# Performance work log

Measured on AMD Instinct MI355X. Metric: run time of the kernel, lower is better.

The kernel has to match this reference:

```python
import jax, jax.numpy as jnp
import numpy as np

N = 100000
E = 1600000


def _gcn_conv(x, src, dst, norm, W, b, n_nodes):
    # PyG GCNConv: h = x @ W; aggregate normalized messages; add bias.
    h = x @ W                                   # [N, C_out]
    msg = h[src] * norm[:, None]                # [E', C_out] gathered messages
    out = jax.ops.segment_sum(msg, dst, num_segments=n_nodes)
    return out + b


def _norm_coeffs(src, dst, n_nodes):
    # symmetric normalization with self-loops: D^{-1/2} (A+I) D^{-1/2}
    ones = jnp.ones(src.shape[0], dtype=jnp.float32)
    deg = jax.ops.segment_sum(ones, dst, num_segments=n_nodes)
    dis = jnp.where(deg > 0, jax.lax.rsqrt(jnp.maximum(deg, 1.0)), 0.0)
    return dis[src] * dis[dst]


def setup_inputs() -> dict:
    key = jax.random.key(0)
    k1, k2, k3, k4 = jax.random.split(key, 4)
    x = jax.random.normal(k1, (N, 128), dtype=jnp.float32)
    edge_index = jax.random.randint(k2, (2, E), 0, N, dtype=jnp.int64)
    W1 = jax.random.normal(k3, (128, 128), dtype=jnp.float32) * (1.0 / np.sqrt(128))
    b1 = jnp.zeros((128,), dtype=jnp.float32)
    W2 = jax.random.normal(k4, (128, 64), dtype=jnp.float32) * (1.0 / np.sqrt(128))
    b2 = jnp.zeros((64,), dtype=jnp.float32)
    return {"x": x, "edge_index": edge_index, "W1": W1, "b1": b1, "W2": W2, "b2": b2}


def reference(x, edge_index, W1, b1, W2, b2):
    n_nodes = x.shape[0]
    loop = jnp.arange(n_nodes, dtype=edge_index.dtype)
    src = jnp.concatenate([edge_index[0], loop])   # add self-loops
    dst = jnp.concatenate([edge_index[1], loop])
    norm = _norm_coeffs(src, dst, n_nodes)
    h = _gcn_conv(x, src, dst, norm, W1, b1, n_nodes)
    h = jax.nn.relu(h)
    # dropout(p=0.2) is identity in eval mode
    out = _gcn_conv(h, src, dst, norm, W2, b2, n_nodes)
    return out
```

## Files before the change

kernel.cpp:

```cpp
#include <hip/hip_runtime.h>
#include <hip/hip_bf16.h>


typedef short short8v __attribute__((ext_vector_type(8)));
typedef float f32x4   __attribute__((ext_vector_type(4)));

#define BSHIFT 9
#define BSIZE  512
#define CAPSH  14
#define CAP    (1 << CAPSH)

__device__ __forceinline__ short f2bf(float f) {
    unsigned u = __float_as_uint(f);
    return (short)((u + 0x7fffu + ((u >> 16) & 1u)) >> 16);
}
__device__ __forceinline__ float bfbits(unsigned short s) {
    return __uint_as_float((unsigned)s << 16);
}
__device__ __forceinline__ unsigned pack2bf(float a, float b) {
    return (unsigned)(unsigned short)f2bf(a) | ((unsigned)(unsigned short)f2bf(b) << 16);
}

__global__ void k_init(int* __restrict__ bcur, int nbuck) {
    int i = threadIdx.x;
    if (i < nbuck) bcur[i] = i << CAPSH;
}

__global__ __launch_bounds__(256) void k_bucket(const int* __restrict__ src,
                                                const int* __restrict__ dst,
                                                int* __restrict__ bcur,
                                                int2* __restrict__ ebuf,
                                                int E, int nbuck) {
    __shared__ int sdst[4096];
    __shared__ int ssrc[4096];
    __shared__ int hist[256];
    __shared__ int base[256];
    int t = threadIdx.x;
    int e0 = blockIdx.x * 4096;
    for (int i = t; i < nbuck; i += 256) hist[i] = 0;
    for (int i = 0; i < 16; ++i) {
        int k = i * 256 + t;
        int e = e0 + k;
        sdst[k] = (e < E) ? dst[e] : -1;
        ssrc[k] = (e < E) ? src[e] : 0;
    }
    __syncthreads();
    for (int i = 0; i < 16; ++i) {
        int d = sdst[i * 256 + t];
        if (d >= 0) atomicAdd(&hist[d >> BSHIFT], 1);
    }
    __syncthreads();
    for (int b = t; b < nbuck; b += 256) {
        int c = hist[b];
        base[b] = c ? atomicAdd(&bcur[b], c) : 0;
        hist[b] = 0;
    }
    __syncthreads();
    for (int i = 0; i < 16; ++i) {
        int k = i * 256 + t;
        int d = sdst[k];
        if (d >= 0) {
            int bk = d >> BSHIFT;
            int off = atomicAdd(&hist[bk], 1);
            ebuf[base[bk] + off] = make_int2(ssrc[k], d);
        }
    }
}

__global__ __launch_bounds__(BSIZE) void k_bdeg(const int2* __restrict__ ebuf,
                                                const int* __restrict__ bcur,
                                                int* __restrict__ deg,
                                                int* __restrict__ row_ptr,
                                                float* __restrict__ dinv, int n) {
    __shared__ int hist[BSIZE];
    __shared__ int s[BSIZE];
    int b = blockIdx.x;
    int t = threadIdx.x;
    hist[t] = 0;
    __syncthreads();
    int base = b << CAPSH;
    int cnt  = bcur[b] - base;
    int lo = b << BSHIFT;
    for (int k = t; k < cnt; k += BSIZE)
        atomicAdd(&hist[ebuf[base + k].y - lo], 1);
    __syncthreads();
    int v = hist[t];
    s[t] = v;
    __syncthreads();
    for (int off = 1; off < BSIZE; off <<= 1) {
        int add = (t >= off) ? s[t - off] : 0;
        __syncthreads();
        s[t] += add;
        __syncthreads();
    }
    int node = lo + t;
    if (node < n) {
        deg[node]     = v;
        row_ptr[node] = base + s[t] - v;
        dinv[node]    = rsqrtf((float)(v + 1));
    }
}

__global__ __launch_bounds__(BSIZE) void k_bscatter(const int2* __restrict__ ebuf,
                                                    const int* __restrict__ bcur,
                                                    const int* __restrict__ row_ptr,
                                                    const float* __restrict__ dinv,
                                                    int2* __restrict__ csr8, int n) {
    __shared__ int cur[BSIZE];
    int b = blockIdx.x;
    int t = threadIdx.x;
    int lo = b << BSHIFT;
    int node = lo + t;
    cur[t] = (node < n) ? row_ptr[node] : 0;
    __syncthreads();
    int base = b << CAPSH;
    int cnt  = bcur[b] - base;
    for (int k = t; k < cnt; k += BSIZE) {
        int2 ed = ebuf[base + k];
        int pos = atomicAdd(&cur[ed.y - lo], 1);
        csr8[pos] = make_int2(ed.x, __float_as_int(dinv[ed.x]));
    }
}

__global__ void k_prepW(const float* __restrict__ W1, const float* __restrict__ W2,
                        short* __restrict__ w1t, short* __restrict__ w2t) {
    int i = blockIdx.x * blockDim.x + threadIdx.x;
    if (i < 128 * 128) {
        int n = i >> 7, k = i & 127;
        w1t[i] = f2bf(W1[k * 128 + n]);
    } else if (i < 128 * 128 + 64 * 128) {
        int j = i - 128 * 128;
        int n = j >> 7, k = j & 127;
        w2t[j] = f2bf(W2[k * 64 + n]);
    }
}

#define LDP 136
__global__ __launch_bounds__(256) void k_gemm1(const float* __restrict__ x,
                                               const short* __restrict__ w1t,
                                               short* __restrict__ h, int nrows) {
    __shared__ short xs[64 * LDP];
    __shared__ short wt[128 * LDP];
    int t = threadIdx.x;
    int row0 = blockIdx.x * 64;
    for (int i = 0; i < 16; ++i) {
        int idx = t + i * 256;
        int r = idx >> 5, c4 = idx & 31;
        float4 v = make_float4(0.f, 0.f, 0.f, 0.f);
        if (row0 + r < nrows) v = ((const float4*)x)[(size_t)(row0 + r) * 32 + c4];
        short4 o = make_short4(f2bf(v.x), f2bf(v.y), f2bf(v.z), f2bf(v.w));
        *(short4*)&xs[r * LDP + c4 * 4] = o;
    }
    for (int i = 0; i < 16; ++i) {
        int idx = t + i * 256;
        int n = idx >> 5, c4 = idx & 31;
        *(short4*)&wt[n * LDP + c4 * 4] = ((const short4*)w1t)[idx];
    }
    __syncthreads();
    int wave = t >> 6, lane = t & 63;
    int quad = lane >> 4, c = lane & 15;
    int m0 = wave * 16;
    f32x4 acc[8] = {};
    #pragma unroll
    for (int kc = 0; kc < 4; ++kc) {
        short8v a = *(const short8v*)&xs[(m0 + c) * LDP + kc * 32 + quad * 8];
        #pragma unroll
        for (int nt = 0; nt < 8; ++nt) {
            short8v b = *(const short8v*)&wt[(nt * 16 + c) * LDP + kc * 32 + quad * 8];
            acc[nt] = __builtin_amdgcn_mfma_f32_16x16x32_bf16(a, b, acc[nt], 0, 0, 0);
        }
    }
    #pragma unroll
    for (int nt = 0; nt < 8; ++nt)
        #pragma unroll
        for (int r = 0; r < 4; ++r) {
            int row = row0 + m0 + quad * 4 + r;
            if (row < nrows) h[(size_t)row * 128 + nt * 16 + c] = f2bf(acc[nt][r]);
        }
}

__global__ __launch_bounds__(256) void k_gemm2(const unsigned* __restrict__ aggb,
                                               const float* __restrict__ b1,
                                               const short* __restrict__ w2t,
                                               short* __restrict__ h2, int nrows) {
    __shared__ short xs[64 * LDP];
    __shared__ short wt[64 * LDP];
    int t = threadIdx.x;
    int row0 = blockIdx.x * 64;
    for (int i = 0; i < 16; ++i) {
        int idx = t + i * 256;
        int r = idx >> 6, cp = idx & 63;
        unsigned o = 0;
        if (row0 + r < nrows) {
            unsigned u = aggb[(size_t)(row0 + r) * 64 + cp];
            float2 bb = ((const float2*)b1)[cp];
            float vx = fmaxf(__uint_as_float(u << 16) + bb.x, 0.f);
            float vy = fmaxf(__uint_as_float(u & 0xffff0000u) + bb.y, 0.f);
            o = pack2bf(vx, vy);
        }
        *(unsigned*)&xs[r * LDP + cp * 2] = o;
    }
    for (int i = 0; i < 8; ++i) {
        int idx = t + i * 256;
        int n = idx >> 5, c4 = idx & 31;
        *(short4*)&wt[n * LDP + c4 * 4] = ((const short4*)w2t)[idx];
    }
    __syncthreads();
    int wave = t >> 6, lane = t & 63;
    int quad = lane >> 4, c = lane & 15;
    int m0 = wave * 16;
    f32x4 acc[4] = {};
    #pragma unroll
    for (int kc = 0; kc < 4; ++kc) {
        short8v av = *(const short8v*)&xs[(m0 + c) * LDP + kc * 32 + quad * 8];
        #pragma unroll
        for (int nt = 0; nt < 4; ++nt) {
            short8v b = *(const short8v*)&wt[(nt * 16 + c) * LDP + kc * 32 + quad * 8];
            acc[nt] = __builtin_amdgcn_mfma_f32_16x16x32_bf16(av, b, acc[nt], 0, 0, 0);
        }
    }
    #pragma unroll
    for (int nt = 0; nt < 4; ++nt)
        #pragma unroll
        for (int r = 0; r < 4; ++r) {
            int row = row0 + m0 + quad * 4 + r;
            if (row < nrows) h2[(size_t)row * 64 + nt * 16 + c] = f2bf(acc[nt][r]);
        }
}

__global__ __launch_bounds__(256) void k_pull128(const unsigned short* __restrict__ h,
                                                 const int* __restrict__ row_ptr,
                                                 const int* __restrict__ deg,
                                                 const int2* __restrict__ csr8,
                                                 const float* __restrict__ dinv,
                                                 unsigned* __restrict__ aggb, int n) {
    int wave = (blockIdx.x * 256 + threadIdx.x) >> 6;
    int lane = threadIdx.x & 63;
    if (wave >= n) return;
    int i = __builtin_amdgcn_readfirstlane(wave);
    float di = dinv[i];
    float2 acc;
    {
        unsigned u = ((const unsigned*)(h + (size_t)i * 128))[lane];
        float w = di * di;
        acc.x = __uint_as_float(u << 16) * w;
        acc.y = __uint_as_float(u & 0xffff0000u) * w;
    }
    int beg = row_ptr[i];
    int cnt = deg[i];
    int k = 0;
    for (; k + 8 <= cnt; k += 8) {
        int2 e[8];
        unsigned u[8];
        #pragma unroll
        for (int j = 0; j < 8; ++j) e[j] = csr8[beg + k + j];
        #pragma unroll
        for (int j = 0; j < 8; ++j)
            u[j] = ((const unsigned*)(h + (size_t)e[j].x * 128))[lane];
        #pragma unroll
        for (int j = 0; j < 8; ++j) {
            float nr = di * __int_as_float(e[j].y);
            acc.x += __uint_as_float(u[j] << 16) * nr;
            acc.y += __uint_as_float(u[j] & 0xffff0000u) * nr;
        }
    }
    for (; k < cnt; ++k) {
        int2 e = csr8[beg + k];
        float nr = di * __int_as_float(e.y);
        unsigned u = ((const unsigned*)(h + (size_t)e.x * 128))[lane];
        acc.x += __uint_as_float(u << 16) * nr;
        acc.y += __uint_as_float(u & 0xffff0000u) * nr;
    }
    aggb[(size_t)i * 64 + lane] = pack2bf(acc.x, acc.y);
}

__global__ __launch_bounds__(256) void k_pull64(const unsigned short* __restrict__ h,
                                                const int* __restrict__ row_ptr,
                                                const int* __restrict__ deg,
                                                const int2* __restrict__ csr8,
                                                const float* __restrict__ dinv,
                                                const float* __restrict__ b2,
                                                float* __restrict__ out, int n) {
    int wave = (blockIdx.x * 256 + threadIdx.x) >> 6;
    int lane = threadIdx.x & 63;
    if (wave >= n) return;
    int i = __builtin_amdgcn_readfirstlane(wave);
    float di = dinv[i];
    float acc = bfbits(h[(size_t)i * 64 + lane]) * di * di;
    int beg = row_ptr[i];
    int cnt = deg[i];
    int k = 0;
    for (; k + 8 <= cnt; k += 8) {
        int2 e[8];
        unsigned short u[8];
        #pragma unroll
        for (int j = 0; j < 8; ++j) e[j] = csr8[beg + k + j];
        #pragma unroll
        for (int j = 0; j < 8; ++j) u[j] = h[(size_t)e[j].x * 64 + lane];
        #pragma unroll
        for (int j = 0; j < 8; ++j)
            acc += bfbits(u[j]) * (di * __int_as_float(e[j].y));
    }
    for (; k < cnt; ++k) {
        int2 e = csr8[beg + k];
        acc += bfbits(h[(size_t)e.x * 64 + lane]) * (di * __int_as_float(e.y));
    }
    out[(size_t)i * 64 + lane] = acc + b2[lane];
}

extern "C" void kernel_launch(void* const* d_in, const int* in_sizes, int n_in,
                              void* d_out, int out_size, void* d_ws, size_t ws_size,
                              hipStream_t stream) {
    const float* x  = (const float*)d_in[0];
    const int*   ei = (const int*)d_in[1];
    const float* W1 = (const float*)d_in[2];
    const float* b1 = (const float*)d_in[3];
    const float* W2 = (const float*)d_in[4];
    const float* b2 = (const float*)d_in[5];
    float* out = (float*)d_out;

    const int N = in_sizes[0] / 128;
    const int E = in_sizes[1] / 2;
    const int* src = ei;
    const int* dst = ei + E;
    const int nbuck = (N + BSIZE - 1) >> BSHIFT;
    const size_t capE = (size_t)nbuck << CAPSH;

    float* dinv    = (float*)d_ws;
    int*   deg     = (int*)(dinv + N);
    int*   row_ptr = deg + N;
    int*   bcur    = row_ptr + N;
    short* w1t     = (short*)(bcur + 256);
    short* w2t     = w1t + 128 * 128;
    int2*  csr8    = (int2*)(w2t + 64 * 128);
    short* bufH    = (short*)(csr8 + capE);
    short* bufH2   = bufH + (size_t)N * 128;
    unsigned* aggb = (unsigned*)(bufH2 + (size_t)N * 64);
    int2*  ebuf    = (int2*)bufH2;

    const int ntile = (E + 4095) / 4096;

    k_init<<<1, 256, 0, stream>>>(bcur, nbuck);
    k_bucket<<<ntile, 256, 0, stream>>>(src, dst, bcur, ebuf, E, nbuck);
    k_bdeg<<<nbuck, BSIZE, 0, stream>>>(ebuf, bcur, deg, row_ptr, dinv, N);
    k_bscatter<<<nbuck, BSIZE, 0, stream>>>(ebuf, bcur, row_ptr, dinv, csr8, N);

    k_prepW<<<96, 256, 0, stream>>>(W1, W2, w1t, w2t);

    k_gemm1<<<(N + 63) / 64, 256, 0, stream>>>(x, w1t, bufH, N);
    k_pull128<<<(N + 3) / 4, 256, 0, stream>>>((const unsigned short*)bufH, row_ptr, deg, csr8, dinv, aggb, N);

    k_gemm2<<<(N + 63) / 64, 256, 0, stream>>>(aggb, b1, w2t, bufH2, N);
    k_pull64<<<(N + 3) / 4, 256, 0, stream>>>((const unsigned short*)bufH2, row_ptr, deg, csr8, dinv, b2, out, N);
}
```

Baseline: 304.5 us.

## Pack edges to 32-bit, fuse CSR build in LDS, look up dinv at pull time

Bucketed edges are now packed into one 32-bit word (source shifted left, plus the local destination), which halves bucket-buffer traffic. The degree and scatter kernels are merged into one kernel that caches each bucket's edges in 64KB of shared memory, so the second global read of the bucket disappears. CSR entries shrink from int2 to a plain source index, and the pull kernels gather dinv[src] with an extra dependent load. Weight prep and bucket-cursor init are merged into a single launch. The costs are higher shared-memory use, which lowers occupancy in the CSR kernel, and an extra random gather per edge in both aggregations.

Measured after the change: 306.9 us. About the same (+0.8%).

```diff
diff --git a/kernel.cpp b/kernel.cpp
--- a/kernel.cpp
+++ b/kernel.cpp
@@ -14,22 +14,36 @@
     unsigned u = __float_as_uint(f);
     return (short)((u + 0x7fffu + ((u >> 16) & 1u)) >> 16);
 }
-__device__ __forceinline__ float bfbits(unsigned short s) {
-    return __uint_as_float((unsigned)s << 16);
-}
 __device__ __forceinline__ unsigned pack2bf(float a, float b) {
     return (unsigned)(unsigned short)f2bf(a) | ((unsigned)(unsigned short)f2bf(b) << 16);
 }
-
-__global__ void k_init(int* __restrict__ bcur, int nbuck) {
-    int i = threadIdx.x;
-    if (i < nbuck) bcur[i] = i << CAPSH;
+__device__ __forceinline__ float bflo(unsigned u) { return __uint_as_float(u << 16); }
+__device__ __forceinline__ float bfhi(unsigned u) { return __uint_as_float(u & 0xffff0000u); }
+
+__global__ void k_prep(const float* __restrict__ W1, const float* __restrict__ W2,
+                       short* __restrict__ w1t, short* __restrict__ w2t,
+                       int* __restrict__ bcur, int nbuck) {
+    int b = blockIdx.x;
+    int t = threadIdx.x;
+    if (b == gridDim.x - 1) {
+        if (t < nbuck) bcur[t] = t << CAPSH;
+        return;
+    }
+    int i = b * 256 + t;
+    if (i < 128 * 128) {
+        int n = i >> 7, k = i & 127;
+        w1t[i] = f2bf(W1[k * 128 + n]);
+    } else {
+        int j = i - 128 * 128;
+        int n = j >> 7, k = j & 127;
+        w2t[j] = f2bf(W2[k * 64 + n]);
+    }
 }
 
 __global__ __launch_bounds__(256) void k_bucket(const int* __restrict__ src,
                                                 const int* __restrict__ dst,
                                                 int* __restrict__ bcur,
-                                                int2* __restrict__ ebuf,
+                                                unsigned* __restrict__ ebuf,
                                                 int E, int nbuck) {
     __shared__ int sdst[4096];
     __shared__ int ssrc[4096];
@@ -62,18 +76,21 @@
         if (d >= 0) {
             int bk = d >> BSHIFT;
             int off = atomicAdd(&hist[bk], 1);
-            ebuf[base[bk] + off] = make_int2(ssrc[k], d);
-        }
-    }
-}
-
-__global__ __launch_bounds__(BSIZE) void k_bdeg(const int2* __restrict__ ebuf,
+            ebuf[base[bk] + off] = ((unsigned)ssrc[k] << BSHIFT) | (unsigned)(d & (BSIZE - 1));
+        }
+    }
+}
+
+__global__ __launch_bounds__(BSIZE) void k_bcsr(const unsigned* __restrict__ ebuf,
                                                 const int* __restrict__ bcur,
                                                 int* __restrict__ deg,
                                                 int* __restrict__ row_ptr,
-                                                float* __restrict__ dinv, int n) {
+                                                float* __restrict__ dinv,
+                                                unsigned* __restrict__ csr4, int n) {
+    __shared__ unsigned edges[CAP];
     __shared__ int hist[BSIZE];
     __shared__ int s[BSIZE];
+    __shared__ int cur[BSIZE];
     int b = blockIdx.x;
     int t = threadIdx.x;
     hist[t] = 0;
@@ -81,8 +98,11 @@
     int base = b << CAPSH;
     int cnt  = bcur[b] - base;
     int lo = b << BSHIFT;
-    for (int k = t; k < cnt; k += BSIZE)
-        atomicAdd(&hist[ebuf[base + k].y - lo], 1);
+    for (int k = t; k < cnt; k += BSIZE) {
+        unsigned e = ebuf[base + k];
+        edges[k] = e;
+        atomicAdd(&hist[e & (BSIZE - 1)], 1);
+    }
     __syncthreads();
     int v = hist[t];
     s[t] = v;
@@ -93,45 +113,19 @@
         s[t] += add;
         __syncthreads();
     }
+    int rp = base + s[t] - v;
+    cur[t] = rp;
     int node = lo + t;
     if (node < n) {
         deg[node]     = v;
-        row_ptr[node] = base + s[t] - v;
+        row_ptr[node] = rp;
         dinv[node]    = rsqrtf((float)(v + 1));
     }
-}
-
-__global__ __launch_bounds__(BSIZE) void k_bscatter(const int2* __restrict__ ebuf,
-                                                    const int* __restrict__ bcur,
-                                                    const int* __restrict__ row_ptr,
-                                                    const float* __restrict__ dinv,
-                                                    int2* __restrict__ csr8, int n) {
-    __shared__ int cur[BSIZE];
-    int b = blockIdx.x;
-    int t = threadIdx.x;
-    int lo = b << BSHIFT;
-    int node = lo + t;
-    cur[t] = (node < n) ? row_ptr[node] : 0;
-    __syncthreads();
-    int base = b << CAPSH;
-    int cnt  = bcur[b] - base;
+    __syncthreads();
     for (int k = t; k < cnt; k += BSIZE) {
-        int2 ed = ebuf[base + k];
-        int pos = atomicAdd(&cur[ed.y - lo], 1);
-        csr8[pos] = make_int2(ed.x, __float_as_int(dinv[ed.x]));
-    }
-}
-
-__global__ void k_prepW(const float* __restrict__ W1, const float* __restrict__ W2,
-                        short* __restrict__ w1t, short* __restrict__ w2t) {
-    int i = blockIdx.x * blockDim.x + threadIdx.x;
-    if (i < 128 * 128) {
-        int n = i >> 7, k = i & 127;
-        w1t[i] = f2bf(W1[k * 128 + n]);
-    } else if (i < 128 * 128 + 64 * 128) {
-        int j = i - 128 * 128;
-        int n = j >> 7, k = j & 127;
-        w2t[j] = f2bf(W2[k * 64 + n]);
+        unsigned e = edges[k];
+        int pos = atomicAdd(&cur[e & (BSIZE - 1)], 1);
+        csr4[pos] = e >> BSHIFT;
     }
 }
 
@@ -194,8 +188,8 @@
         if (row0 + r < nrows) {
             unsigned u = aggb[(size_t)(row0 + r) * 64 + cp];
             float2 bb = ((const float2*)b1)[cp];
-            float vx = fmaxf(__uint_as_float(u << 16) + bb.x, 0.f);
-            float vy = fmaxf(__uint_as_float(u & 0xffff0000u) + bb.y, 0.f);
+            float vx = fmaxf(bflo(u) + bb.x, 0.f);
+            float vy = fmaxf(bfhi(u) + bb.y, 0.f);
             o = pack2bf(vx, vy);
         }
         *(unsigned*)&xs[r * LDP + cp * 2] = o;
@@ -231,7 +225,7 @@
 __global__ __launch_bounds__(256) void k_pull128(const unsigned short* __restrict__ h,
                                                  const int* __restrict__ row_ptr,
                                                  const int* __restrict__ deg,
-                                                 const int2* __restrict__ csr8,
+                                                 const unsigned* __restrict__ csr4,
                                                  const float* __restrict__ dinv,
                                                  unsigned* __restrict__ aggb, int n) {
     int wave = (blockIdx.x * 256 + threadIdx.x) >> 6;
@@ -243,33 +237,36 @@
     {
         unsigned u = ((const unsigned*)(h + (size_t)i * 128))[lane];
         float w = di * di;
-        acc.x = __uint_as_float(u << 16) * w;
-        acc.y = __uint_as_float(u & 0xffff0000u) * w;
+        acc.x = bflo(u) * w;
+        acc.y = bfhi(u) * w;
     }
     int beg = row_ptr[i];
     int cnt = deg[i];
     int k = 0;
     for (; k + 8 <= cnt; k += 8) {
-        int2 e[8];
-        unsigned u[8];
-        #pragma unroll
-        for (int j = 0; j < 8; ++j) e[j] = csr8[beg + k + j];
+        unsigned sid[8];
+        float ds[8];
+        unsigned g[8];
+        #pragma unroll
+        for (int j = 0; j < 8; ++j) sid[j] = csr4[beg + k + j];
+        #pragma unroll
+        for (int j = 0; j < 8; ++j) ds[j] = dinv[sid[j]];
         #pragma unroll
         for (int j = 0; j < 8; ++j)
-            u[j] = ((const unsigned*)(h + (size_t)e[j].x * 128))[lane];
+            g[j] = ((const unsigned*)(h + (size_t)sid[j] * 128))[lane];
         #pragma unroll
         for (int j = 0; j < 8; ++j) {
-            float nr = di * __int_as_float(e[j].y);
-            acc.x += __uint_as_float(u[j] << 16) * nr;
-            acc.y += __uint_as_float(u[j] & 0xffff0000u) * nr;
+            float nr = di * ds[j];
+            acc.x += bflo(g[j]) * nr;
+            acc.y += bfhi(g[j]) * nr;
         }
     }
     for (; k < cnt; ++k) {
-        int2 e = csr8[beg + k];
-        float nr = di * __int_as_float(e.y);
-        unsigned u = ((const unsigned*)(h + (size_t)e.x * 128))[lane];
-        acc.x += __uint_as_float(u << 16) * nr;
-        acc.y += __uint_as_float(u & 0xffff0000u) * nr;
+        unsigned sid = csr4[beg + k];
+        float nr = di * dinv[sid];
+        unsigned g = ((const unsigned*)(h + (size_t)sid * 128))[lane];
+        acc.x += bflo(g) * nr;
+        acc.y += bfhi(g) * nr;
     }
     aggb[(size_t)i * 64 + lane] = pack2bf(acc.x, acc.y);
 }
@@ -277,7 +274,7 @@
 __global__ __launch_bounds__(256) void k_pull64(const unsigned short* __restrict__ h,
                                                 const int* __restrict__ row_ptr,
                                                 const int* __restrict__ deg,
-                                                const int2* __restrict__ csr8,
+                                                const unsigned* __restrict__ csr4,
                                                 const float* __restrict__ dinv,
                                                 const float* __restrict__ b2,
                                                 float* __restrict__ out, int n) {
@@ -286,24 +283,31 @@
     if (wave >= n) return;
     int i = __builtin_amdgcn_readfirstlane(wave);
     float di = dinv[i];
-    float acc = bfbits(h[(size_t)i * 64 + lane]) * di * di;
+    float acc = bflo((unsigned)h[(size_t)i * 64 + lane] << 16 >> 16 << 16) * 0.0f;
+    {
+        unsigned u = h[(size_t)i * 64 + lane];
+        acc = __uint_as_float(u << 16) * di * di;
+    }
     int beg = row_ptr[i];
     int cnt = deg[i];
     int k = 0;
     for (; k + 8 <= cnt; k += 8) {
-        int2 e[8];
+        unsigned sid[8];
+        float ds[8];
         unsigned short u[8];
         #pragma unroll
-        for (int j = 0; j < 8; ++j) e[j] = csr8[beg + k + j];
-        #pragma unroll
-        for (int j = 0; j < 8; ++j) u[j] = h[(size_t)e[j].x * 64 + lane];
+        for (int j = 0; j < 8; ++j) sid[j] = csr4[beg + k + j];
+        #pragma unroll
+        for (int j = 0; j < 8; ++j) ds[j] = dinv[sid[j]];
+        #pragma unroll
+        for (int j = 0; j < 8; ++j) u[j] = h[(size_t)sid[j] * 64 + lane];
         #pragma unroll
         for (int j = 0; j < 8; ++j)
-            acc += bfbits(u[j]) * (di * __int_as_float(e[j].y));
+            acc += __uint_as_float((unsigned)u[j] << 16) * (di * ds[j]);
     }
     for (; k < cnt; ++k) {
-        int2 e = csr8[beg + k];
-        acc += bfbits(h[(size_t)e.x * 64 + lane]) * (di * __int_as_float(e.y));
+        unsigned sid = csr4[beg + k];
+        acc += __uint_as_float((unsigned)h[(size_t)sid * 64 + lane] << 16) * (di * dinv[sid]);
     }
     out[(size_t)i * 64 + lane] = acc + b2[lane];
 }
@@ -326,30 +330,28 @@
     const int nbuck = (N + BSIZE - 1) >> BSHIFT;
     const size_t capE = (size_t)nbuck << CAPSH;
 
-    float* dinv    = (float*)d_ws;
-    int*   deg     = (int*)(dinv + N);
-    int*   row_ptr = deg + N;
-    int*   bcur    = row_ptr + N;
-    short* w1t     = (short*)(bcur + 256);
-    short* w2t     = w1t + 128 * 128;
-    int2*  csr8    = (int2*)(w2t + 64 * 128);
-    short* bufH    = (short*)(csr8 + capE);
-    short* bufH2   = bufH + (size_t)N * 128;
-    unsigned* aggb = (unsigned*)(bufH2 + (size_t)N * 64);
-    int2*  ebuf    = (int2*)bufH2;
+    float* dinv     = (float*)d_ws;
+    int*   deg      = (int*)(dinv + N);
+    int*   row_ptr  = deg + N;
+    int*   bcur     = row_ptr + N;
+    short* w1t      = (short*)(bcur + 256);
+    short* w2t      = w1t + 128 * 128;
+    unsigned* csr4  = (unsigned*)(w2t + 64 * 128);
+    short* bufH     = (short*)(csr4 + capE);
+    short* bufH2    = bufH + (size_t)N * 128;
+    unsigned* aggb  = (unsigned*)(bufH2 + (size_t)N * 64);
+    unsigned* ebuf  = (unsigned*)bufH2;
 
     const int ntile = (E + 4095) / 4096;
 
-    k_init<<<1, 256, 0, stream>>>(bcur, nbuck);
+    k_prep<<<97, 256, 0, stream>>>(W1, W2, w1t, w2t, bcur, nbuck);
+
     k_bucket<<<ntile, 256, 0, stream>>>(src, dst, bcur, ebuf, E, nbuck);
-    k_bdeg<<<nbuck, BSIZE, 0, stream>>>(ebuf, bcur, deg, row_ptr, dinv, N);
-    k_bscatter<<<nbuck, BSIZE, 0, stream>>>(ebuf, bcur, row_ptr, dinv, csr8, N);
-
-    k_prepW<<<96, 256, 0, stream>>>(W1, W2, w1t, w2t);
+    k_bcsr<<<nbuck, BSIZE, 0, stream>>>(ebuf, bcur, deg, row_ptr, dinv, csr4, N);
 
     k_gemm1<<<(N + 63) / 64, 256, 0, stream>>>(x, w1t, bufH, N);
-    k_pull128<<<(N + 3) / 4, 256, 0, stream>>>((const unsigned short*)bufH, row_ptr, deg, csr8, dinv, aggb, N);
+    k_pull128<<<(N + 3) / 4, 256, 0, stream>>>((const unsigned short*)bufH, row_ptr, deg, csr4, dinv, aggb, N);
 
     k_gemm2<<<(N + 63) / 64, 256, 0, stream>>>(aggb, b1, w2t, bufH2, N);
-    k_pull64<<<(N + 3) / 4, 256, 0, stream>>>((const unsigned short*)bufH2, row_ptr, deg, csr8, dinv, b2, out, N);
-}
+    k_pull64<<<(N + 3) / 4, 256, 0, stream>>>((const unsigned short*)bufH2, row_ptr, deg, csr4, dinv, b2, out, N);
+}
```
